# Performance work log

Hardware: AMD Instinct MI355X
Metric: run time of the kernel (lower is better)

## Reference

```python
import jax, jax.numpy as jnp
import numpy as np


def _bilinear_sample(img, y, x):
    # img: [B,C,H,W]; y, x: [B,Gh,Gw] float sampling coords (pixel units)
    B, C, H, W = img.shape
    y0 = jnp.floor(y)
    x0 = jnp.floor(x)
    wy1 = y - y0
    wx1 = x - x0
    wy0 = 1.0 - wy1
    wx0 = 1.0 - wx1
    flat = img.reshape(B, C, H * W)

    def gather(yi, xi):
        valid = (yi >= 0) & (yi <= H - 1) & (xi >= 0) & (xi <= W - 1)
        yc = jnp.clip(yi, 0, H - 1).astype(jnp.int32)
        xc = jnp.clip(xi, 0, W - 1).astype(jnp.int32)
        idx = (yc * W + xc).reshape(B, 1, -1)  # [B,1,Gh*Gw]
        g = jnp.take_along_axis(flat, jnp.broadcast_to(idx, (B, C, idx.shape[-1])), axis=2)
        g = g.reshape(B, C, yi.shape[1], yi.shape[2])
        return g * valid[:, None].astype(img.dtype)

    out = (gather(y0, x0) * (wy0 * wx0)[:, None]
           + gather(y0, x0 + 1) * (wy0 * wx1)[:, None]
           + gather(y0 + 1, x0) * (wy1 * wx0)[:, None]
           + gather(y0 + 1, x0 + 1) * (wy1 * wx1)[:, None])
    return out


def setup_inputs() -> dict:
    key = jax.random.key(0)
    k1, k2 = jax.random.split(key)
    B, C, H, W = 32, 64, 128, 128
    Gh, Gw = 64, 64
    x = jax.random.normal(k1, (B, C, H, W), dtype=jnp.float32)
    offset = jax.random.normal(k2, (B, 2, Gh, Gw), dtype=jnp.float32)
    return {"x": x, "offset": offset, "grid_h": Gh, "grid_w": Gw, "shift": 0}


def reference(x, offset, grid_h, grid_w, shift):
    # Deformable feature-map resampling: sample input at a regular grid of
    # size (grid_h, grid_w) scaled to the input extent, shifted by `shift`,
    # displaced by learned per-location offsets (dy, dx), bilinear interp,
    # zeros outside bounds. Output: [B, C, grid_h, grid_w].
    B, C, H, W = x.shape
    scale_h = H / grid_h
    scale_w = W / grid_w
    gy = jnp.arange(grid_h, dtype=x.dtype) * scale_h + shift  # [Gh]
    gx = jnp.arange(grid_w, dtype=x.dtype) * scale_w + shift  # [Gw]
    y = gy[None, :, None] + offset[:, 0]  # [B,Gh,Gw]
    xx = gx[None, None, :] + offset[:, 1]  # [B,Gh,Gw]
    return _bilinear_sample(x, y, xx)
```

## Files before the change

kernel.cpp:

```cpp
#include <hip/hip_runtime.h>

#define BB 32
#define CC 64
#define HH 128
#define WW 128
#define GH 64
#define GW 64
#define PLANE (HH * WW)
#define OUTP  (GH * GW)
#define CPB 4

__device__ __forceinline__ void stage_plane(const float* __restrict__ src,
                                            float* dst, int tid) {
    #pragma unroll
    for (int k = 0; k < 4; ++k) {
        const int fo = k * 4096 + tid * 4;
        __builtin_amdgcn_global_load_lds(
            (const __attribute__((address_space(1))) void*)(src + fo),
            (__attribute__((address_space(3))) void*)(dst + fo),
            16, 0, 0);
    }
}

__global__ __launch_bounds__(1024) void defem_kernel(
    const float* __restrict__ x,
    const float* __restrict__ off,
    const int* __restrict__ shift_p,
    float* __restrict__ out)
{
    __shared__ float lds[2 * PLANE];

    const int tid = threadIdx.x;
    const int blk = blockIdx.x;
    const int b   = blk >> 4;
    const int c0  = (blk & 15) * CPB;

    const float* __restrict__ src0 = x + (size_t)(b * CC + c0) * PLANE;
    const float* __restrict__ offb = off + (size_t)b * 2 * OUTP;
    float* __restrict__ out0 = out + (size_t)(b * CC + c0) * OUTP;

    stage_plane(src0, lds, tid);

    const float shift = (float)shift_p[0];
    int rA[4], rB[4];
    float u0a[4], u0b[4], u1a[4], u1b[4];

    #pragma unroll
    for (int k = 0; k < 4; ++k) {
        const int s  = k * 1024 + tid;
        const int gw = s & (GW - 1);
        const int gh = s >> 6;

        const float dy = offb[s];
        const float dx = offb[OUTP + s];

        const float y  = (float)gh * 2.0f + shift + dy;
        const float xx = (float)gw * 2.0f + shift + dx;

        const float y0f = floorf(y);
        const float x0f = floorf(xx);
        const float wy1 = y - y0f;
        const float wx1 = xx - x0f;
        const float wy0 = 1.0f - wy1;
        const float wx0 = 1.0f - wx1;
        const int y0 = (int)y0f;
        const int x0 = (int)x0f;
        const int y1 = y0 + 1;
        const int x1 = x0 + 1;

        const float vy0 = (y0 >= 0 && y0 < HH) ? 1.0f : 0.0f;
        const float vy1 = (y1 >= 0 && y1 < HH) ? 1.0f : 0.0f;
        const float vx0 = (x0 >= 0 && x0 < WW) ? 1.0f : 0.0f;
        const float vx1 = (x1 >= 0 && x1 < WW) ? 1.0f : 0.0f;

        const float w00 = wy0 * wx0 * vy0 * vx0;
        const float w01 = wy0 * wx1 * vy0 * vx1;
        const float w10 = wy1 * wx0 * vy1 * vx0;
        const float w11 = wy1 * wx1 * vy1 * vx1;

        const int yc0 = min(max(y0, 0), HH - 1);
        const int yc1 = min(max(y1, 0), HH - 1);
        const int xs  = min(max(x0, 0), WW - 2);
        const bool sel = (x0 == xs);

        u0a[k] = sel ? w00 : w01;
        u0b[k] = sel ? w01 : w00;
        u1a[k] = sel ? w10 : w11;
        u1b[k] = sel ? w11 : w10;
        rA[k] = yc0 * WW + xs;
        rB[k] = yc1 * WW + xs;
    }

    __syncthreads();

    #pragma unroll
    for (int p = 0; p < CPB; ++p) {
        if (p + 1 < CPB)
            stage_plane(src0 + (size_t)(p + 1) * PLANE,
                        lds + ((p + 1) & 1) * PLANE, tid);

        const float* __restrict__ pl = lds + (p & 1) * PLANE;
        float* __restrict__ ob = out0 + (size_t)p * OUTP;

        #pragma unroll
        for (int k = 0; k < 4; ++k) {
            const int s = k * 1024 + tid;
            const float a0 = pl[rA[k]];
            const float a1 = pl[rA[k] + 1];
            const float b0 = pl[rB[k]];
            const float b1 = pl[rB[k] + 1];
            ob[s] = a0 * u0a[k] + a1 * u0b[k] + b0 * u1a[k] + b1 * u1b[k];
        }

        __syncthreads();
    }
}

extern "C" void kernel_launch(void* const* d_in, const int* in_sizes, int n_in,
                              void* d_out, int out_size, void* d_ws, size_t ws_size,
                              hipStream_t stream) {
    const float* x   = (const float*)d_in[0];
    const float* off = (const float*)d_in[1];
    const int* shift_p = (const int*)d_in[4];
    float* out = (float*)d_out;

    const int grid = BB * CC / CPB;
    defem_kernel<<<grid, 1024, 0, stream>>>(x, off, shift_p, out);
}
```

Baseline: 33.41 us.

## Replace async LDS double buffer with register-staged single plane buffer

Drops the global_load_lds double-buffered staging and instead prefetches the next plane into registers (float4), then writes it to a single 64KB LDS plane after the compute and a barrier. Halving LDS use from 128KB to 64KB per block may let more blocks per CU be resident on parts with 160KB LDS. The trade-off is an extra barrier per plane, higher register pressure, and serialized LDS writes instead of direct async copies.

```diff
diff --git a/kernel.cpp b/kernel.cpp
--- a/kernel.cpp
+++ b/kernel.cpp
@@ -10,25 +10,13 @@
 #define OUTP  (GH * GW)
 #define CPB 4
 
-__device__ __forceinline__ void stage_plane(const float* __restrict__ src,
-                                            float* dst, int tid) {
-    #pragma unroll
-    for (int k = 0; k < 4; ++k) {
-        const int fo = k * 4096 + tid * 4;
-        __builtin_amdgcn_global_load_lds(
-            (const __attribute__((address_space(1))) void*)(src + fo),
-            (__attribute__((address_space(3))) void*)(dst + fo),
-            16, 0, 0);
-    }
-}
-
 __global__ __launch_bounds__(1024) void defem_kernel(
     const float* __restrict__ x,
     const float* __restrict__ off,
     const int* __restrict__ shift_p,
     float* __restrict__ out)
 {
-    __shared__ float lds[2 * PLANE];
+    __shared__ float plane[PLANE];
 
     const int tid = threadIdx.x;
     const int blk = blockIdx.x;
@@ -39,7 +27,10 @@
     const float* __restrict__ offb = off + (size_t)b * 2 * OUTP;
     float* __restrict__ out0 = out + (size_t)(b * CC + c0) * OUTP;
 
-    stage_plane(src0, lds, tid);
+    float4 st[4];
+    #pragma unroll
+    for (int k = 0; k < 4; ++k)
+        st[k] = *(const float4*)(src0 + k * 4096 + tid * 4);
 
     const float shift = (float)shift_p[0];
     int rA[4], rB[4];
@@ -91,28 +82,39 @@
         rB[k] = yc1 * WW + xs;
     }
 
+    #pragma unroll
+    for (int k = 0; k < 4; ++k)
+        *(float4*)(plane + k * 4096 + tid * 4) = st[k];
     __syncthreads();
 
-    #pragma unroll
+    #pragma unroll 1
     for (int p = 0; p < CPB; ++p) {
-        if (p + 1 < CPB)
-            stage_plane(src0 + (size_t)(p + 1) * PLANE,
-                        lds + ((p + 1) & 1) * PLANE, tid);
+        if (p + 1 < CPB) {
+            const float* __restrict__ srcn = src0 + (size_t)(p + 1) * PLANE;
+            #pragma unroll
+            for (int k = 0; k < 4; ++k)
+                st[k] = *(const float4*)(srcn + k * 4096 + tid * 4);
+        }
 
-        const float* __restrict__ pl = lds + (p & 1) * PLANE;
         float* __restrict__ ob = out0 + (size_t)p * OUTP;
-
         #pragma unroll
         for (int k = 0; k < 4; ++k) {
             const int s = k * 1024 + tid;
-            const float a0 = pl[rA[k]];
-            const float a1 = pl[rA[k] + 1];
-            const float b0 = pl[rB[k]];
-            const float b1 = pl[rB[k] + 1];
+            const float a0 = plane[rA[k]];
+            const float a1 = plane[rA[k] + 1];
+            const float b0 = plane[rB[k]];
+            const float b1 = plane[rB[k] + 1];
             ob[s] = a0 * u0a[k] + a1 * u0b[k] + b0 * u1a[k] + b1 * u1b[k];
         }
 
         __syncthreads();
+
+        if (p + 1 < CPB) {
+            #pragma unroll
+            for (int k = 0; k < 4; ++k)
+                *(float4*)(plane + k * 4096 + tid * 4) = st[k];
+            __syncthreads();
+        }
     }
 }
 
```

New measurement: 63.53 us. 90.2% more time.

## Process one channel plane per block instead of double-buffered four-channel blocks

Applied to the files above, without the earlier changes.

Each block now stages a single 64KB input plane into LDS and computes one output channel. The four-channel in-block double-buffered pipeline is removed. Halving LDS per block allows two resident blocks per CU, so overlap comes from concurrent blocks rather than explicit prefetch. The trade-off is that sampling weights and offsets are recomputed for every channel instead of being amortized over four.

```diff
diff --git a/kernel.cpp b/kernel.cpp
--- a/kernel.cpp
+++ b/kernel.cpp
@@ -8,38 +8,30 @@
 #define GW 64
 #define PLANE (HH * WW)
 #define OUTP  (GH * GW)
-#define CPB 4
 
-__device__ __forceinline__ void stage_plane(const float* __restrict__ src,
-                                            float* dst, int tid) {
+__global__ __launch_bounds__(1024, 8) void defem_kernel(
+    const float* __restrict__ x,
+    const float* __restrict__ off,
+    const int* __restrict__ shift_p,
+    float* __restrict__ out)
+{
+    __shared__ float plane[PLANE];
+
+    const int tid = threadIdx.x;
+    const int blk = blockIdx.x;
+    const int b   = blk >> 6;
+
+    const float* __restrict__ src  = x + (size_t)blk * PLANE;
+    const float* __restrict__ offb = off + (size_t)b * 2 * OUTP;
+
     #pragma unroll
     for (int k = 0; k < 4; ++k) {
         const int fo = k * 4096 + tid * 4;
         __builtin_amdgcn_global_load_lds(
             (const __attribute__((address_space(1))) void*)(src + fo),
-            (__attribute__((address_space(3))) void*)(dst + fo),
+            (__attribute__((address_space(3))) void*)(plane + fo),
             16, 0, 0);
     }
-}
-
-__global__ __launch_bounds__(1024) void defem_kernel(
-    const float* __restrict__ x,
-    const float* __restrict__ off,
-    const int* __restrict__ shift_p,
-    float* __restrict__ out)
-{
-    __shared__ float lds[2 * PLANE];
-
-    const int tid = threadIdx.x;
-    const int blk = blockIdx.x;
-    const int b   = blk >> 4;
-    const int c0  = (blk & 15) * CPB;
-
-    const float* __restrict__ src0 = x + (size_t)(b * CC + c0) * PLANE;
-    const float* __restrict__ offb = off + (size_t)b * 2 * OUTP;
-    float* __restrict__ out0 = out + (size_t)(b * CC + c0) * OUTP;
-
-    stage_plane(src0, lds, tid);
 
     const float shift = (float)shift_p[0];
     int rA[4], rB[4];
@@ -93,26 +85,16 @@
 
     __syncthreads();
 
+    float* __restrict__ obase = out + (size_t)blk * OUTP;
+
     #pragma unroll
-    for (int p = 0; p < CPB; ++p) {
-        if (p + 1 < CPB)
-            stage_plane(src0 + (size_t)(p + 1) * PLANE,
-                        lds + ((p + 1) & 1) * PLANE, tid);
-
-        const float* __restrict__ pl = lds + (p & 1) * PLANE;
-        float* __restrict__ ob = out0 + (size_t)p * OUTP;
-
-        #pragma unroll
-        for (int k = 0; k < 4; ++k) {
-            const int s = k * 1024 + tid;
-            const float a0 = pl[rA[k]];
-            const float a1 = pl[rA[k] + 1];
-            const float b0 = pl[rB[k]];
-            const float b1 = pl[rB[k] + 1];
-            ob[s] = a0 * u0a[k] + a1 * u0b[k] + b0 * u1a[k] + b1 * u1b[k];
-        }
-
-        __syncthreads();
+    for (int k = 0; k < 4; ++k) {
+        const int s = k * 1024 + tid;
+        const float a0 = plane[rA[k]];
+        const float a1 = plane[rA[k] + 1];
+        const float b0 = plane[rB[k]];
+        const float b1 = plane[rB[k] + 1];
+        obase[s] = a0 * u0a[k] + a1 * u0b[k] + b0 * u1a[k] + b1 * u1b[k];
     }
 }
 
@@ -124,6 +106,6 @@
     const int* shift_p = (const int*)d_in[4];
     float* out = (float*)d_out;
 
-    const int grid = BB * CC / CPB;
+    const int grid = BB * CC;
     defem_kernel<<<grid, 1024, 0, stream>>>(x, off, shift_p, out);
 }
```

Measured after the change: 31.06 us. 7.0% less time.
